# Optimization experiments

Measured on AMD Instinct MI355X. Metric: run time of the kernel, lower is better.

## Reference

```python
import jax, jax.numpy as jnp
import numpy as np

N, E = 32768, 8192            # num_nodes, num_hyperedges
ND, ED, HD, OD, NH = 128, 128, 64, 128, 4  # node/edge/hidden/output dims, heads
EPS = 1e-8


def min_max_normalize(x):
    # per-feature (column-wise) min-max normalization, as in utils.min_max_normalize_cuda
    mn = x.min(axis=0)
    mx = x.max(axis=0)
    return (x - mn) / (mx - mn + EPS)


def setup_inputs() -> dict:
    key = jax.random.key(0)
    ks = jax.random.split(key, 12)
    s = 0.05
    node_features = jax.random.normal(ks[0], (N, ND), jnp.float32)
    # sparse-ish binary incidence matrix stored dense (as the torch code uses dense mm)
    incidence_matrix = (jax.random.uniform(ks[1], (N, E)) < 0.01).astype(jnp.float32)
    edge_features = jax.random.normal(ks[2], (E, ED), jnp.float32)
    # stacked per-head parameters (heads are chained, so head input dim == ND == OD)
    nodeW = jax.random.normal(ks[3], (NH, ND, HD), jnp.float32) * s
    nodeB = jnp.zeros((NH, HD), jnp.float32)
    edgeW = jax.random.normal(ks[4], (NH, ED, HD), jnp.float32) * s
    edgeB = jnp.zeros((NH, HD), jnp.float32)
    attnW = jax.random.normal(ks[5], (NH, HD, 1), jnp.float32) * s
    attnB = jnp.zeros((NH, 1), jnp.float32)
    outW = jax.random.normal(ks[6], (NH, HD, OD), jnp.float32) * s
    outB = jnp.zeros((NH, OD), jnp.float32)
    return dict(node_features=node_features, incidence_matrix=incidence_matrix,
                edge_features=edge_features, nodeW=nodeW, nodeB=nodeB,
                edgeW=edgeW, edgeB=edgeB, attnW=attnW, attnB=attnB,
                outW=outW, outB=outB)


def reference(node_features, incidence_matrix, edge_features,
              nodeW, nodeB, edgeW, edgeB, attnW, attnB, outW, outB):
    # node degree normalizer, shared across heads
    deg = incidence_matrix.sum(axis=1, keepdims=True) + EPS  # [N, 1]
    x = node_features
    for h in range(NH):  # heads are applied sequentially (chained), per original forward
        tn = x @ nodeW[h] + nodeB[h]                       # [N, HD]
        te = edge_features @ edgeW[h] + edgeB[h]           # [E, HD]
        agg = (incidence_matrix @ te) / deg                # [N, HD] mean over incident edges
        scores = (tn + agg) @ attnW[h] + attnB[h]          # [N, 1]
        scores = jnp.where(scores >= 0, scores, 0.2 * scores)  # LeakyReLU(0.2)
        coeffs = jax.nn.sigmoid(scores)                    # [N, 1]
        upd = coeffs * agg + tn                            # gated residual
        upd = upd @ outW[h] + outB[h]                      # [N, OD]
        upd = min_max_normalize(upd)
        x = jax.nn.relu(upd)                               # ReLU applied after each head
    # dropout is identity at inference; output_transform is defined but never used
    return x
```

## Files before the change

kernel.cpp:

```cpp
#include <hip/hip_runtime.h>
#include <cstdint>
#include <cstddef>

#define N_NODES 32768
#define N_EDGES 8192
#define ND 128
#define HD 64
#define OD 128
#define NH 4
#define EPSV 1e-8f

#define WPB 4
#define CAP 512
#define LCAP 16

__device__ __forceinline__ unsigned encf(float f) {
  unsigned b = __float_as_uint(f);
  return (b & 0x80000000u) ? ~b : (b | 0x80000000u);
}
__device__ __forceinline__ float decf(unsigned u) {
  unsigned b = (u & 0x80000000u) ? (u & 0x7fffffffu) : ~u;
  return __uint_as_float(b);
}

__global__ __launch_bounds__(256) void k_prep(
    const float* __restrict__ inc, const float* __restrict__ ef,
    float* __restrict__ P, float* __restrict__ deg)
{
  __shared__ int s_seg[WPB][64][LCAP];
  __shared__ __align__(16) int s_dense[WPB][CAP];
  const int t = threadIdx.x;
  const int lane = t & 63;
  const int wv = t >> 6;
  const int node = blockIdx.x * WPB + wv;
  const float* row = inc + (size_t)node * N_EDGES + lane * 4;

  float4 r[8];
  #pragma unroll
  for (int i = 0; i < 8; i++) r[i] = *(const float4*)(row + i * 256);
  int c = 0;
  #pragma unroll
  for (int o = 0; o < 4; o++) {
    #pragma unroll
    for (int i = 0; i < 8; i++) {
      const float4 v = r[i];
      const int nx = (o + 1) * 8 + i;
      if (nx < 32) r[i] = *(const float4*)(row + nx * 256);
      const int col0 = (o * 8 + i) * 256 + lane * 4;
      if (v.x != 0.f) { s_seg[wv][lane][c & (LCAP - 1)] = col0 + 0; c++; }
      if (v.y != 0.f) { s_seg[wv][lane][c & (LCAP - 1)] = col0 + 1; c++; }
      if (v.z != 0.f) { s_seg[wv][lane][c & (LCAP - 1)] = col0 + 2; c++; }
      if (v.w != 0.f) { s_seg[wv][lane][c & (LCAP - 1)] = col0 + 3; c++; }
    }
  }

  int pre = c;
  #pragma unroll
  for (int o = 1; o < 64; o <<= 1) {
    const int tv = __shfl_up(pre, o, 64);
    if (lane >= o) pre += tv;
  }
  const int total0 = __shfl(pre, 63, 64);
  const int excl = pre - c;
  if (lane == 0) deg[node] = (float)total0 + EPSV;

  const int cc = (c < LCAP) ? c : LCAP;
  for (int i = 0; i < cc; i++) {
    const int p = excl + i;
    if (p < CAP) s_dense[wv][p] = s_seg[wv][lane][i];
  }
  const int total = (total0 < CAP) ? total0 : CAP;

  const float* efl = ef + lane;
  float acc0 = 0.f, acc1 = 0.f;
  int i = 0;
  for (; i + 4 <= total; i += 4) {
    const int4 cs = *(const int4*)&s_dense[wv][i];
    const float a0 = efl[(size_t)cs.x * ND], b0 = efl[(size_t)cs.x * ND + 64];
    const float a1 = efl[(size_t)cs.y * ND], b1 = efl[(size_t)cs.y * ND + 64];
    const float a2 = efl[(size_t)cs.z * ND], b2 = efl[(size_t)cs.z * ND + 64];
    const float a3 = efl[(size_t)cs.w * ND], b3 = efl[(size_t)cs.w * ND + 64];
    acc0 += (a0 + a1) + (a2 + a3);
    acc1 += (b0 + b1) + (b2 + b3);
  }
  for (; i < total; i++) {
    const int cx = s_dense[wv][i];
    acc0 += efl[(size_t)cx * ND];
    acc1 += efl[(size_t)cx * ND + 64];
  }
  P[(size_t)node * ND + lane] = acc0;
  P[(size_t)node * ND + 64 + lane] = acc1;
}

__global__ __launch_bounds__(512, 4) void k_head(
    const float* __restrict__ xin, const float* __restrict__ P,
    const float* __restrict__ deg,
    const float* __restrict__ nodeW, const float* __restrict__ nodeB,
    const float* __restrict__ edgeW, const float* __restrict__ edgeB,
    const float* __restrict__ attnW, const float* __restrict__ attnB,
    const float* __restrict__ outW, const float* __restrict__ outB,
    const unsigned* __restrict__ pmn, const unsigned* __restrict__ pmx,
    unsigned* __restrict__ omn, unsigned* __restrict__ omx,
    float* __restrict__ y, const int do_norm)
{
  constexpr int LDW = 129;
  __shared__ float xs[64 * LDW];
  __shared__ float ps[64 * LDW];
  __shared__ float s_att[8 * 64];
  const int t = threadIdx.x;
  const int r0 = blockIdx.x * 64;
  const int lane = t & 63;
  const int wv = __builtin_amdgcn_readfirstlane(t >> 6);
  const int j0 = wv * 8;

  float4 xv[4], pv[4];
  int rowi[4], c4i[4];
  #pragma unroll
  for (int i = 0; i < 4; i++) {
    const int f = t + i * 512;
    rowi[i] = f >> 5;
    c4i[i] = (f & 31) * 4;
    xv[i] = *(const float4*)(xin + (size_t)(r0 + rowi[i]) * ND + c4i[i]);
  }
  #pragma unroll
  for (int i = 0; i < 4; i++)
    pv[i] = *(const float4*)(P + (size_t)(r0 + rowi[i]) * ND + c4i[i]);

  asm volatile("s_waitcnt vmcnt(4)" ::: "memory");

  #pragma unroll
  for (int i = 0; i < 4; i++) {
    float xa[4] = {xv[i].x, xv[i].y, xv[i].z, xv[i].w};
    if (do_norm) {
      #pragma unroll
      for (int c = 0; c < 4; c++) {
        const float mn = decf(pmn[c4i[i] + c]);
        const float mx = decf(pmx[c4i[i] + c]);
        const float v = (xa[c] - mn) / (mx - mn + EPSV);
        xa[c] = v > 0.f ? v : 0.f;
      }
    }
    #pragma unroll
    for (int c = 0; c < 4; c++) xs[rowi[i] * LDW + c4i[i] + c] = xa[c];
  }
  __syncthreads();

  float tn[8];
  #pragma unroll
  for (int j = 0; j < 8; j++) tn[j] = 0.f;
  const float* xrow = &xs[lane * LDW];
  #pragma unroll 4
  for (int k = 0; k < ND; k++) {
    const float xvv = xrow[k];
    const float* nw = nodeW + (size_t)k * HD + j0;
    #pragma unroll
    for (int j = 0; j < 8; j++) tn[j] = fmaf(xvv, nw[j], tn[j]);
  }

  asm volatile("s_waitcnt vmcnt(0)" ::: "memory");
  #pragma unroll
  for (int i = 0; i < 4; i++) {
    ps[rowi[i] * LDW + c4i[i] + 0] = pv[i].x;
    ps[rowi[i] * LDW + c4i[i] + 1] = pv[i].y;
    ps[rowi[i] * LDW + c4i[i] + 2] = pv[i].z;
    ps[rowi[i] * LDW + c4i[i] + 3] = pv[i].w;
  }
  const float d = deg[r0 + lane];
  __syncthreads();

  float agg[8];
  #pragma unroll
  for (int j = 0; j < 8; j++) agg[j] = 0.f;
  const float* prow = &ps[lane * LDW];
  #pragma unroll 4
  for (int k = 0; k < ND; k++) {
    const float pvv = prow[k];
    const float* ew = edgeW + (size_t)k * HD + j0;
    #pragma unroll
    for (int j = 0; j < 8; j++) agg[j] = fmaf(pvv, ew[j], agg[j]);
  }

  const float rsum = d - EPSV;
  const float inv_d = 1.f / d;
  float sp = 0.f;
  #pragma unroll
  for (int j = 0; j < 8; j++) {
    const float tj = tn[j] + nodeB[j0 + j];
    const float aj = fmaf(rsum, edgeB[j0 + j], agg[j]) * inv_d;
    tn[j] = tj;
    agg[j] = aj;
    sp = fmaf(tj + aj, attnW[j0 + j], sp);
  }
  s_att[wv * 64 + lane] = sp;
  __syncthreads();
  float s = attnB[0];
  #pragma unroll
  for (int w = 0; w < 8; w++) s += s_att[w * 64 + lane];
  s = (s >= 0.f) ? s : 0.2f * s;
  const float coeff = 1.f / (1.f + expf(-s));

  float* us = ps;
  #pragma unroll
  for (int j = 0; j < 8; j++) {
    us[lane * 65 + j0 + j] = fmaf(coeff, agg[j], tn[j]);
  }
  __syncthreads();

  const int jo0 = wv * 16;
  float yacc[16];
  #pragma unroll
  for (int i = 0; i < 16; i++) yacc[i] = outB[jo0 + i];
  #pragma unroll 4
  for (int k = 0; k < HD; k++) {
    const float uv = us[lane * 65 + k];
    const float* ow = outW + (size_t)k * OD + jo0;
    #pragma unroll
    for (int i = 0; i < 16; i++) yacc[i] = fmaf(uv, ow[i], yacc[i]);
  }

  float* ys = xs;
  #pragma unroll
  for (int i = 0; i < 16; i++) ys[lane * LDW + jo0 + i] = yacc[i];
  __syncthreads();
  #pragma unroll
  for (int i = 0; i < 4; i++) {
    const float4 o = make_float4(ys[rowi[i] * LDW + c4i[i] + 0],
                                 ys[rowi[i] * LDW + c4i[i] + 1],
                                 ys[rowi[i] * LDW + c4i[i] + 2],
                                 ys[rowi[i] * LDW + c4i[i] + 3]);
    *(float4*)(y + (size_t)(r0 + rowi[i]) * OD + c4i[i]) = o;
  }
  const int col = jo0 + (lane & 15);
  const int rg = lane >> 4;
  float lo = 3.4e38f, hi = -3.4e38f;
  #pragma unroll
  for (int i = 0; i < 16; i++) {
    const float v = ys[(rg + 4 * i) * LDW + col];
    lo = fminf(lo, v);
    hi = fmaxf(hi, v);
  }
  lo = fminf(lo, __shfl_xor(lo, 16, 64));
  hi = fmaxf(hi, __shfl_xor(hi, 16, 64));
  lo = fminf(lo, __shfl_xor(lo, 32, 64));
  hi = fmaxf(hi, __shfl_xor(hi, 32, 64));
  if (rg == 0) {
    atomicMin(&omn[col], encf(lo));
    atomicMax(&omx[col], encf(hi));
  }
}

__global__ __launch_bounds__(256) void k_final(
    const float* __restrict__ y, const unsigned* __restrict__ mn_enc,
    const unsigned* __restrict__ mx_enc, float* __restrict__ out)
{
  const int i = blockIdx.x * 256 + threadIdx.x;
  const int col = i & (OD - 1);
  const float mn = decf(mn_enc[col]);
  const float mx = decf(mx_enc[col]);
  const float v = (y[i] - mn) / (mx - mn + EPSV);
  out[i] = (v > 0.f) ? v : 0.f;
}

extern "C" void kernel_launch(void* const* d_in, const int* in_sizes, int n_in,
                              void* d_out, int out_size, void* d_ws, size_t ws_size,
                              hipStream_t stream)
{
  const float* node_features = (const float*)d_in[0];
  const float* incidence     = (const float*)d_in[1];
  const float* edge_features = (const float*)d_in[2];
  const float* nodeW = (const float*)d_in[3];
  const float* nodeB = (const float*)d_in[4];
  const float* edgeW = (const float*)d_in[5];
  const float* edgeB = (const float*)d_in[6];
  const float* attnW = (const float*)d_in[7];
  const float* attnB = (const float*)d_in[8];
  const float* outW  = (const float*)d_in[9];
  const float* outB  = (const float*)d_in[10];
  float* out = (float*)d_out;

  float* P   = (float*)d_ws;
  float* yA  = P + (size_t)N_NODES * ND;
  float* yB  = yA + (size_t)N_NODES * OD;
  float* deg = yB + (size_t)N_NODES * OD;
  unsigned* mn = (unsigned*)(deg + N_NODES);
  unsigned* mx = mn + NH * OD;

  hipMemsetAsync(mn, 0xFF, NH * OD * sizeof(unsigned), stream);
  hipMemsetAsync(mx, 0x00, NH * OD * sizeof(unsigned), stream);

  k_prep<<<N_NODES / WPB, 256, 0, stream>>>(incidence, edge_features, P, deg);

  float* ybuf[2] = {yA, yB};
  for (int h = 0; h < NH; h++) {
    const float* xin = (h == 0) ? node_features : ybuf[(h + 1) & 1];
    float* yout = ybuf[h & 1];
    const unsigned* pmn = (h == 0) ? mn : mn + (size_t)(h - 1) * OD;
    const unsigned* pmx = (h == 0) ? mx : mx + (size_t)(h - 1) * OD;
    k_head<<<N_NODES / 64, 512, 0, stream>>>(
        xin, P, deg,
        nodeW + (size_t)h * ND * HD, nodeB + (size_t)h * HD,
        edgeW + (size_t)h * ND * HD, edgeB + (size_t)h * HD,
        attnW + (size_t)h * HD, attnB + h,
        outW + (size_t)h * HD * OD, outB + (size_t)h * OD,
        pmn, pmx, mn + (size_t)h * OD, mx + (size_t)h * OD,
        yout, (h > 0) ? 1 : 0);
  }
  k_final<<<(N_NODES * OD) / 256, 256, 0, stream>>>(
      ybuf[(NH - 1) & 1], mn + (size_t)(NH - 1) * OD, mx + (size_t)(NH - 1) * OD, out);
}
```

Before: 1.596 ms.

## Precompute per-head edge transforms and gather them instead of raw edge features

Adds a kernel that computes te = edge_features @ edgeW + edgeB for all four heads up front. The prep kernel then gathers and sums 64-wide te rows per head instead of 128-wide raw features, writing per-head aggregates. Each head kernel no longer runs the 128x64 edge projection per node, which removes that per-head matmul work. In exchange the gather reads four head arrays per incident edge, and the workspace grows to hold te and four aggregate arrays.

```diff
diff --git a/kernel.cpp b/kernel.cpp
--- a/kernel.cpp
+++ b/kernel.cpp
@@ -23,9 +23,49 @@
   return __uint_as_float(b);
 }
 
+__global__ __launch_bounds__(512) void k_te(
+    const float* __restrict__ ef, const float* __restrict__ edgeW,
+    const float* __restrict__ edgeB, float* __restrict__ te)
+{
+  constexpr int LDW = 129;
+  __shared__ float es[64 * LDW];
+  const int nb = N_EDGES / 64;
+  const int h  = blockIdx.x / nb;
+  const int e0 = (blockIdx.x % nb) * 64;
+  const int t = threadIdx.x;
+  const int lane = t & 63;
+  const int wv = __builtin_amdgcn_readfirstlane(t >> 6);
+  #pragma unroll
+  for (int i = 0; i < 4; i++) {
+    const int f = t + i * 512;
+    const int row = f >> 5;
+    const int c4 = (f & 31) * 4;
+    const float4 v = *(const float4*)(ef + (size_t)(e0 + row) * ND + c4);
+    es[row * LDW + c4 + 0] = v.x; es[row * LDW + c4 + 1] = v.y;
+    es[row * LDW + c4 + 2] = v.z; es[row * LDW + c4 + 3] = v.w;
+  }
+  __syncthreads();
+  const int j0 = wv * 8;
+  const float* eW = edgeW + (size_t)h * ND * HD;
+  float acc[8];
+  #pragma unroll
+  for (int j = 0; j < 8; j++) acc[j] = edgeB[h * HD + j0 + j];
+  const float* erow = &es[lane * LDW];
+  #pragma unroll 4
+  for (int k = 0; k < ND; k++) {
+    const float v = erow[k];
+    const float* w = eW + (size_t)k * HD + j0;
+    #pragma unroll
+    for (int j = 0; j < 8; j++) acc[j] = fmaf(v, w[j], acc[j]);
+  }
+  float* dst = te + ((size_t)h * N_EDGES + e0 + lane) * HD + j0;
+  *(float4*)(dst + 0) = make_float4(acc[0], acc[1], acc[2], acc[3]);
+  *(float4*)(dst + 4) = make_float4(acc[4], acc[5], acc[6], acc[7]);
+}
+
 __global__ __launch_bounds__(256) void k_prep(
-    const float* __restrict__ inc, const float* __restrict__ ef,
-    float* __restrict__ P, float* __restrict__ deg)
+    const float* __restrict__ inc, const float* __restrict__ te,
+    float* __restrict__ AGG, float* __restrict__ deg)
 {
   __shared__ int s_seg[WPB][64][LCAP];
   __shared__ __align__(16) int s_dense[WPB][CAP];
@@ -71,32 +111,36 @@
   }
   const int total = (total0 < CAP) ? total0 : CAP;
 
-  const float* efl = ef + lane;
-  float acc0 = 0.f, acc1 = 0.f;
+  const float* t0p = te + lane;
+  const float* t1p = t0p + (size_t)N_EDGES * HD;
+  const float* t2p = t1p + (size_t)N_EDGES * HD;
+  const float* t3p = t2p + (size_t)N_EDGES * HD;
+  float a0 = 0.f, a1 = 0.f, a2 = 0.f, a3 = 0.f;
   int i = 0;
-  for (; i + 4 <= total; i += 4) {
-    const int4 cs = *(const int4*)&s_dense[wv][i];
-    const float a0 = efl[(size_t)cs.x * ND], b0 = efl[(size_t)cs.x * ND + 64];
-    const float a1 = efl[(size_t)cs.y * ND], b1 = efl[(size_t)cs.y * ND + 64];
-    const float a2 = efl[(size_t)cs.z * ND], b2 = efl[(size_t)cs.z * ND + 64];
-    const float a3 = efl[(size_t)cs.w * ND], b3 = efl[(size_t)cs.w * ND + 64];
-    acc0 += (a0 + a1) + (a2 + a3);
-    acc1 += (b0 + b1) + (b2 + b3);
-  }
-  for (; i < total; i++) {
-    const int cx = s_dense[wv][i];
-    acc0 += efl[(size_t)cx * ND];
-    acc1 += efl[(size_t)cx * ND + 64];
-  }
-  P[(size_t)node * ND + lane] = acc0;
-  P[(size_t)node * ND + 64 + lane] = acc1;
+  for (; i + 2 <= total; i += 2) {
+    const int2 c2 = *(const int2*)&s_dense[wv][i];
+    const size_t o0 = (size_t)c2.x * HD, o1 = (size_t)c2.y * HD;
+    const float x00 = t0p[o0], x01 = t0p[o1];
+    const float x10 = t1p[o0], x11 = t1p[o1];
+    const float x20 = t2p[o0], x21 = t2p[o1];
+    const float x30 = t3p[o0], x31 = t3p[o1];
+    a0 += x00 + x01; a1 += x10 + x11;
+    a2 += x20 + x21; a3 += x30 + x31;
+  }
+  if (i < total) {
+    const size_t o0 = (size_t)s_dense[wv][i] * HD;
+    a0 += t0p[o0]; a1 += t1p[o0]; a2 += t2p[o0]; a3 += t3p[o0];
+  }
+  AGG[((size_t)0 * N_NODES + node) * HD + lane] = a0;
+  AGG[((size_t)1 * N_NODES + node) * HD + lane] = a1;
+  AGG[((size_t)2 * N_NODES + node) * HD + lane] = a2;
+  AGG[((size_t)3 * N_NODES + node) * HD + lane] = a3;
 }
 
 __global__ __launch_bounds__(512, 4) void k_head(
-    const float* __restrict__ xin, const float* __restrict__ P,
+    const float* __restrict__ xin, const float* __restrict__ ag,
     const float* __restrict__ deg,
     const float* __restrict__ nodeW, const float* __restrict__ nodeB,
-    const float* __restrict__ edgeW, const float* __restrict__ edgeB,
     const float* __restrict__ attnW, const float* __restrict__ attnB,
     const float* __restrict__ outW, const float* __restrict__ outB,
     const unsigned* __restrict__ pmn, const unsigned* __restrict__ pmx,
@@ -105,7 +149,7 @@
 {
   constexpr int LDW = 129;
   __shared__ float xs[64 * LDW];
-  __shared__ float ps[64 * LDW];
+  __shared__ float as[64 * 65];
   __shared__ float s_att[8 * 64];
   const int t = threadIdx.x;
   const int r0 = blockIdx.x * 64;
@@ -113,7 +157,7 @@
   const int wv = __builtin_amdgcn_readfirstlane(t >> 6);
   const int j0 = wv * 8;
 
-  float4 xv[4], pv[4];
+  float4 xv[4];
   int rowi[4], c4i[4];
   #pragma unroll
   for (int i = 0; i < 4; i++) {
@@ -122,11 +166,18 @@
     c4i[i] = (f & 31) * 4;
     xv[i] = *(const float4*)(xin + (size_t)(r0 + rowi[i]) * ND + c4i[i]);
   }
-  #pragma unroll
-  for (int i = 0; i < 4; i++)
-    pv[i] = *(const float4*)(P + (size_t)(r0 + rowi[i]) * ND + c4i[i]);
-
-  asm volatile("s_waitcnt vmcnt(4)" ::: "memory");
+  float4 av[2];
+  int arow[2], ac4[2];
+  #pragma unroll
+  for (int i = 0; i < 2; i++) {
+    const int f = t + i * 512;
+    arow[i] = f >> 4;
+    ac4[i] = (f & 15) * 4;
+    av[i] = *(const float4*)(ag + (size_t)(r0 + arow[i]) * HD + ac4[i]);
+  }
+  const float d = deg[r0 + lane];
+
+  asm volatile("s_waitcnt vmcnt(3)" ::: "memory");
 
   #pragma unroll
   for (int i = 0; i < 4; i++) {
@@ -159,37 +210,22 @@
 
   asm volatile("s_waitcnt vmcnt(0)" ::: "memory");
   #pragma unroll
-  for (int i = 0; i < 4; i++) {
-    ps[rowi[i] * LDW + c4i[i] + 0] = pv[i].x;
-    ps[rowi[i] * LDW + c4i[i] + 1] = pv[i].y;
-    ps[rowi[i] * LDW + c4i[i] + 2] = pv[i].z;
-    ps[rowi[i] * LDW + c4i[i] + 3] = pv[i].w;
-  }
-  const float d = deg[r0 + lane];
-  __syncthreads();
-
-  float agg[8];
-  #pragma unroll
-  for (int j = 0; j < 8; j++) agg[j] = 0.f;
-  const float* prow = &ps[lane * LDW];
-  #pragma unroll 4
-  for (int k = 0; k < ND; k++) {
-    const float pvv = prow[k];
-    const float* ew = edgeW + (size_t)k * HD + j0;
-    #pragma unroll
-    for (int j = 0; j < 8; j++) agg[j] = fmaf(pvv, ew[j], agg[j]);
-  }
-
-  const float rsum = d - EPSV;
+  for (int i = 0; i < 2; i++) {
+    as[arow[i] * 65 + ac4[i] + 0] = av[i].x;
+    as[arow[i] * 65 + ac4[i] + 1] = av[i].y;
+    as[arow[i] * 65 + ac4[i] + 2] = av[i].z;
+    as[arow[i] * 65 + ac4[i] + 3] = av[i].w;
+  }
+  __syncthreads();
+
   const float inv_d = 1.f / d;
+  float agv[8];
   float sp = 0.f;
   #pragma unroll
   for (int j = 0; j < 8; j++) {
-    const float tj = tn[j] + nodeB[j0 + j];
-    const float aj = fmaf(rsum, edgeB[j0 + j], agg[j]) * inv_d;
-    tn[j] = tj;
-    agg[j] = aj;
-    sp = fmaf(tj + aj, attnW[j0 + j], sp);
+    agv[j] = as[lane * 65 + j0 + j] * inv_d;
+    tn[j] += nodeB[j0 + j];
+    sp = fmaf(tn[j] + agv[j], attnW[j0 + j], sp);
   }
   s_att[wv * 64 + lane] = sp;
   __syncthreads();
@@ -199,10 +235,10 @@
   s = (s >= 0.f) ? s : 0.2f * s;
   const float coeff = 1.f / (1.f + expf(-s));
 
-  float* us = ps;
+  float* us = as;
   #pragma unroll
   for (int j = 0; j < 8; j++) {
-    us[lane * 65 + j0 + j] = fmaf(coeff, agg[j], tn[j]);
+    us[lane * 65 + j0 + j] = fmaf(coeff, agv[j], tn[j]);
   }
   __syncthreads();
 
@@ -278,8 +314,9 @@
   const float* outB  = (const float*)d_in[10];
   float* out = (float*)d_out;
 
-  float* P   = (float*)d_ws;
-  float* yA  = P + (size_t)N_NODES * ND;
+  float* te  = (float*)d_ws;
+  float* AGG = te + (size_t)NH * N_EDGES * HD;
+  float* yA  = AGG + (size_t)NH * N_NODES * HD;
   float* yB  = yA + (size_t)N_NODES * OD;
   float* deg = yB + (size_t)N_NODES * OD;
   unsigned* mn = (unsigned*)(deg + N_NODES);
@@ -288,7 +325,10 @@
   hipMemsetAsync(mn, 0xFF, NH * OD * sizeof(unsigned), stream);
   hipMemsetAsync(mx, 0x00, NH * OD * sizeof(unsigned), stream);
 
-  k_prep<<<N_NODES / WPB, 256, 0, stream>>>(incidence, edge_features, P, deg);
+  k_te<<<NH * (N_EDGES / 64), 512, 0, stream>>>(
+      edge_features, edgeW, edgeB, te);
+
+  k_prep<<<N_NODES / WPB, 256, 0, stream>>>(incidence, te, AGG, deg);
 
   float* ybuf[2] = {yA, yB};
   for (int h = 0; h < NH; h++) {
@@ -297,9 +337,8 @@
     const unsigned* pmn = (h == 0) ? mn : mn + (size_t)(h - 1) * OD;
     const unsigned* pmx = (h == 0) ? mx : mx + (size_t)(h - 1) * OD;
     k_head<<<N_NODES / 64, 512, 0, stream>>>(
-        xin, P, deg,
+        xin, AGG + (size_t)h * N_NODES * HD, deg,
         nodeW + (size_t)h * ND * HD, nodeB + (size_t)h * HD,
-        edgeW + (size_t)h * ND * HD, edgeB + (size_t)h * HD,
         attnW + (size_t)h * HD, attnB + h,
         outW + (size_t)h * HD * OD, outB + (size_t)h * OD,
         pmn, pmx, mn + (size_t)h * OD, mx + (size_t)h * OD,
```

Measured after the change: 1.680 ms. 5.3% more time.
